# Kernel optimization log

Hardware: AMD Instinct MI355X
Metric: run time of the kernel (lower is better)

The kernel has to match this reference:

```python
import jax, jax.numpy as jnp
import numpy as np


def silu(v):
    return v * jax.nn.sigmoid(v)


def setup_inputs() -> dict:
    key = jax.random.key(0)
    ks = jax.random.split(key, 9)
    B, L, d_model = 2, 2048, 1024
    expand, d_state, d_conv = 2, 16, 4
    d_inner = expand * d_model          # 2048
    dt_rank = (d_model + 15) // 16      # 64 (ceil(d_model/16))
    sc = 0.02
    s = lambda k, shape: (jax.random.normal(k, shape, jnp.float32) * sc)
    A_init = jnp.tile(jnp.arange(1, d_state + 1, dtype=jnp.float32), (d_inner, 1))
    return {
        "x": jax.random.normal(ks[0], (B, L, d_model), jnp.float32),
        "in_proj_w": s(ks[1], (2 * d_inner, d_model)),
        "conv_w": s(ks[2], (d_inner, 1, d_conv)),
        "conv_b": s(ks[3], (d_inner,)),
        "x_proj_w": s(ks[4], (dt_rank + 2 * d_state, d_inner)),
        "dt_proj_w": s(ks[5], (d_inner, dt_rank)),
        "dt_proj_b": s(ks[6], (d_inner,)),
        "A_log": jnp.log(A_init),
        "D": jnp.ones((d_inner,), jnp.float32),
        "out_proj_w": s(ks[7], (d_model, d_inner)),
    }


def _mamba(x, in_proj_w, conv_w, conv_b, x_proj_w, dt_proj_w, dt_proj_b, A_log, D, out_proj_w):
    Bsz, L, d_model = x.shape
    d_inner, _, d_conv = conv_w.shape
    d_state = A_log.shape[1]
    dt_rank = dt_proj_w.shape[1]

    # input projection -> [B, L, 2*d_inner], split into conv branch and gate
    xz = jnp.einsum('bld,ed->ble', x, in_proj_w)
    x_in, z = jnp.split(xz, 2, axis=-1)

    # causal depthwise conv1d over sequence
    xt = jnp.transpose(x_in, (0, 2, 1))                      # [B, d_inner, L]
    xt = jnp.pad(xt, ((0, 0), (0, 0), (d_conv - 1, 0)))
    xc = jax.lax.conv_general_dilated(
        xt, conv_w, window_strides=(1,), padding='VALID',
        dimension_numbers=('NCH', 'OIH', 'NCH'),
        feature_group_count=d_inner)
    xc = xc + conv_b[None, :, None]
    u = silu(jnp.transpose(xc, (0, 2, 1)))                   # [B, L, d_inner]

    # ssm parameter projections
    x_dbl = jnp.einsum('ble,fe->blf', u, x_proj_w)           # [B, L, dt_rank + 2*d_state]
    dt, B_ssm, C_ssm = jnp.split(x_dbl, [dt_rank, dt_rank + d_state], axis=-1)
    delta = jax.nn.softplus(jnp.einsum('blr,er->ble', dt, dt_proj_w) + dt_proj_b)  # [B,L,d_inner]
    A = -jnp.exp(A_log)                                       # [d_inner, d_state]

    # selective scan: h_t = exp(delta_t * A) * h_{t-1} + delta_t * u_t * B_t
    def step(h, inp):
        d_t, B_t, C_t, u_t = inp                              # [B,e],[B,n],[B,n],[B,e]
        dA = jnp.exp(d_t[..., None] * A)                      # [B, d_inner, d_state]
        h = dA * h + (d_t * u_t)[..., None] * B_t[:, None, :]
        y = jnp.einsum('ben,bn->be', h, C_t)
        return h, y

    h0 = jnp.zeros((Bsz, d_inner, d_state), x.dtype)
    scan_in = (jnp.swapaxes(delta, 0, 1), jnp.swapaxes(B_ssm, 0, 1),
               jnp.swapaxes(C_ssm, 0, 1), jnp.swapaxes(u, 0, 1))
    _, ys = jax.lax.scan(step, h0, scan_in)                   # ys: [L, B, d_inner]
    y = jnp.swapaxes(ys, 0, 1) + u * D                        # skip term D*u

    y = y * silu(z)                                           # gate
    return jnp.einsum('ble,de->bld', y, out_proj_w)


def reference(x, in_proj_w, conv_w, conv_b, x_proj_w, dt_proj_w, dt_proj_b, A_log, D, out_proj_w):
    # ResidualMamba: x + Mamba(x)
    return x + _mamba(x, in_proj_w, conv_w, conv_b, x_proj_w,
                      dt_proj_w, dt_proj_b, A_log, D, out_proj_w)
```

## Files before the change

### kernel.cpp

```cpp
#include <hip/hip_runtime.h>
#include <hip/hip_bf16.h>
#include <math.h>

typedef __bf16 bf16;
typedef __attribute__((ext_vector_type(8))) __bf16 bf16x8;
typedef __attribute__((ext_vector_type(4))) __bf16 bf16x4;
typedef __attribute__((ext_vector_type(4))) float  f32x4;

static constexpr int Bsz = 2, L = 2048, DM = 1024, DI = 2048, DS = 16, DTR = 64;
static constexpr int M   = Bsz * L;
static constexpr int NXZ = 2 * DI;
static constexpr int NXD = DTR + 2 * DS;
static constexpr int NC  = 32;
static constexpr int CL  = L / NC;
static constexpr int KS  = 8;
static constexpr float LOG2E = 1.4426950408889634f;

__device__ inline float ex2(float x) { return __builtin_amdgcn_exp2f(x); }

__device__ inline void gload_lds16(const void* g, void* l)
{
    __builtin_amdgcn_global_load_lds(
        (const __attribute__((address_space(1))) void*)g,
        (__attribute__((address_space(3))) void*)l, 16, 0, 0);
}

#define SBAR() { asm volatile("" ::: "memory"); __builtin_amdgcn_s_barrier(); asm volatile("" ::: "memory"); }
#define VMCNT12() asm volatile("s_waitcnt vmcnt(12)" ::: "memory")
#define VMCNT9()  asm volatile("s_waitcnt vmcnt(9)" ::: "memory")
#define VMCNT8()  asm volatile("s_waitcnt vmcnt(8)" ::: "memory")
#define VMCNT6()  asm volatile("s_waitcnt vmcnt(6)" ::: "memory")
#define VMCNT4()  asm volatile("s_waitcnt vmcnt(4)" ::: "memory")
#define VMCNT3()  asm volatile("s_waitcnt vmcnt(3)" ::: "memory")
#define VMCNT0()  asm volatile("s_waitcnt vmcnt(0)" ::: "memory")


static constexpr int C0 = M * DM / 4;
static constexpr int C1 = C0 + NXZ * DM / 4;
static constexpr int C2 = C1 + DM * DI / 4;
static constexpr int C3 = C2 + NXD * DI / 4;
static constexpr int C4 = C3 + DI * DTR / 4;

__global__ __launch_bounds__(256)
void cast_all(const float* __restrict__ s0, const float* __restrict__ s1,
              const float* __restrict__ s2, const float* __restrict__ s3,
              const float* __restrict__ s4,
              bf16* __restrict__ d0, bf16* __restrict__ d1,
              bf16* __restrict__ d2, bf16* __restrict__ d3,
              bf16* __restrict__ d4)
{
    const int i = blockIdx.x * 256 + threadIdx.x;
    const float* s; bf16* d; int off;
    if      (i < C0) { s = s0; d = d0; off = 0;  }
    else if (i < C1) { s = s1; d = d1; off = C0; }
    else if (i < C2) { s = s2; d = d2; off = C1; }
    else if (i < C3) { s = s3; d = d3; off = C2; }
    else             { s = s4; d = d4; off = C3; }
    const int j = i - off;
    float4 v = ((const float4*)s)[j];
    bf16x4 o = {(bf16)v.x, (bf16)v.y, (bf16)v.z, (bf16)v.w};
    ((bf16x4*)d)[j] = o;
}

static constexpr int GK  = DM;
static constexpr int GNT = GK / 64;

__device__ __forceinline__ void stage_half(const bf16* __restrict__ Gbase, int ld,
                                           int kbase, bf16* lds_slot, int tid, int wid)
{
    const int rl = tid >> 2;
    const int ks = ((((tid & 3) - ((tid >> 3) & 3)) & 3) << 3);
#pragma unroll
    for (int i = 0; i < 2; ++i)
        gload_lds16(Gbase + (size_t)(i * 128 + rl) * ld + kbase + ks,
                    lds_slot + i * 4096 + wid * 512);
}

template<int MH>
__device__ __forceinline__ void ldA4(const bf16* As, int abase, bf16x8 af[4])
{
#pragma unroll
    for (int mm = 0; mm < 4; ++mm)
        af[mm] = *(const bf16x8*)(As + abase + (MH * 4 + mm) * 512);
}

__device__ __forceinline__ void ldB4(const bf16* Bs, int bbase, bf16x8 bfr[4])
{
#pragma unroll
    for (int nn = 0; nn < 4; ++nn)
        bfr[nn] = *(const bf16x8*)(Bs + bbase + nn * 512);
}

template<int MH>
__device__ __forceinline__ void mfma16(f32x4 acc[8][4], const bf16x8 af[4],
                                       const bf16x8 bfr[4])
{
#pragma unroll
    for (int mm = 0; mm < 4; ++mm)
#pragma unroll
        for (int nn = 0; nn < 4; ++nn)
            acc[MH * 4 + mm][nn] = __builtin_amdgcn_mfma_f32_16x16x32_bf16(
                af[mm], bfr[nn], acc[MH * 4 + mm][nn], 0, 0, 0);
}

__global__ __launch_bounds__(512, 1)
void gemm256_inproj(const bf16* __restrict__ A, const bf16* __restrict__ Bw,
                    bf16* __restrict__ C)
{
    __shared__ __align__(16) bf16 Asl[4 * 8192];
    __shared__ __align__(16) bf16 Bsl[4 * 8192];

    const int tid  = threadIdx.x;
    const int wid  = tid >> 6;
    const int lane = tid & 63;
    const int wr   = wid >> 2;
    const int wc   = wid & 3;
    const int fr   = lane & 15;
    const int ko16 = lane >> 4;
    const int kx   = (((ko16 + ((fr >> 1) & 3)) & 3) << 3);

    const int bid = blockIdx.x;
    const int wg  = (bid & 7) * 32 + (bid >> 3);
    const int by  = wg >> 4, bx = wg & 15;
    const int row0 = by * 256, col0 = bx * 256;

    const bf16* Ablk = A  + (size_t)row0 * GK;
    const bf16* Bblk = Bw + (size_t)col0 * GK;

    const int abase = (wr * 128 + fr) * 32 + kx;
    const int bbase = (wc * 64 + fr) * 32 + kx;

    f32x4 acc[8][4] = {};
    bf16x8 af[4], bfr[4];

    stage_half(Ablk, GK, 0,       Asl + 0 * 8192, tid, wid);
    stage_half(Bblk, GK, 0,       Bsl + 0 * 8192, tid, wid);
    stage_half(Ablk, GK, 32,      Asl + 1 * 8192, tid, wid);
    stage_half(Bblk, GK, 32,      Bsl + 1 * 8192, tid, wid);
    stage_half(Ablk, GK, 64,      Asl + 2 * 8192, tid, wid);
    stage_half(Bblk, GK, 64,      Bsl + 2 * 8192, tid, wid);
    VMCNT4();
    SBAR();

    for (int t = 0; t < GNT; ++t) {
        const int sk0 = (2 * t) & 3, sk1 = (2 * t + 1) & 3;
        const bf16* As0 = Asl + sk0 * 8192;
        const bf16* As1 = Asl + sk1 * 8192;
        const bf16* Bs0 = Bsl + sk0 * 8192;
        const bf16* Bs1 = Bsl + sk1 * 8192;

        ldA4<0>(As0, abase, af);
        ldB4(Bs0, bbase, bfr);
        if (t + 1 < GNT)
            stage_half(Ablk, GK, (t + 1) * 64 + 32, Asl + ((2 * t + 3) & 3) * 8192, tid, wid);
        SBAR();
        __builtin_amdgcn_s_setprio(1);
        mfma16<0>(acc, af, bfr);
        __builtin_amdgcn_s_setprio(0);
        SBAR();

        ldA4<1>(As0, abase, af);
        if (t + 1 < GNT)
            stage_half(Bblk, GK, (t + 1) * 64 + 32, Bsl + ((2 * t + 3) & 3) * 8192, tid, wid);
        SBAR();
        __builtin_amdgcn_s_setprio(1);
        mfma16<1>(acc, af, bfr);
        __builtin_amdgcn_s_setprio(0);
        SBAR();

        ldA4<0>(As1, abase, af);
        ldB4(Bs1, bbase, bfr);
        if (t + 2 < GNT)
            stage_half(Ablk, GK, (t + 2) * 64, Asl + sk0 * 8192, tid, wid);
        SBAR();
        __builtin_amdgcn_s_setprio(1);
        mfma16<0>(acc, af, bfr);
        __builtin_amdgcn_s_setprio(0);
        SBAR();

        ldA4<1>(As1, abase, af);
        if (t + 2 < GNT)
            stage_half(Bblk, GK, (t + 2) * 64, Bsl + sk0 * 8192, tid, wid);
        SBAR();
        __builtin_amdgcn_s_setprio(1);
        mfma16<1>(acc, af, bfr);
        __builtin_amdgcn_s_setprio(0);
        if (t < GNT - 3) { VMCNT4(); } else { VMCNT0(); }
        SBAR();
    }

    const int r0 = row0 + wr * 128 + (ko16 << 2);
    const int c0 = col0 + wc * 64 + fr;
#pragma unroll
    for (int m = 0; m < 8; ++m)
#pragma unroll
        for (int n = 0; n < 4; ++n)
#pragma unroll
            for (int r = 0; r < 4; ++r)
                C[(size_t)(r0 + m * 16 + r) * NXZ + c0 + n * 16] = (bf16)acc[m][n][r];
}

__global__ __launch_bounds__(256)
void gemm_out(const bf16* __restrict__ A, const bf16* __restrict__ Bw,
              const float* __restrict__ res, float* __restrict__ Cout)
{
    __shared__ __align__(16) bf16 Asl[4][128 * 32];
    __shared__ __align__(16) bf16 Bsl[4][64 * 32];

    const int tid  = threadIdx.x;
    const int bid  = blockIdx.x;
    const int orig = (bid & 7) * 64 + (bid >> 3);
    const int bx   = orig & 15;
    const int by   = orig >> 4;
    const int row0 = by * 128, col0 = bx * 64;

    const int w    = tid >> 6;
    const int lane = tid & 63;
    const int wr   = w >> 1, wc = w & 1;
    const int fr   = lane & 15;
    const int ko   = (((lane >> 4) + ((fr >> 1) & 3)) & 3) << 3;

    f32x4 acc[4][2] = {};

    const int sr  = tid >> 2;
    const int ssk = ((((tid & 3) - ((tid >> 3) & 3)) & 3) << 3);
    const bf16* gA0 = A  + (size_t)(row0 + sr) * NXZ + ssk;
    const bf16* gA1 = A  + (size_t)(row0 + 64 + sr) * NXZ + ssk;
    const bf16* gB0 = Bw + (size_t)(col0 + sr) * DI + ssk;

    const int NT = DI / 32;

#define STAGE_OUT(s, kk) do { \
        gload_lds16(gA0 + (kk), (char*)Asl[s] + w * 1024); \
        gload_lds16(gA1 + (kk), (char*)Asl[s] + 4096 + w * 1024); \
        gload_lds16(gB0 + (kk), (char*)Bsl[s] + w * 1024); } while (0)

    STAGE_OUT(0, 0);
    STAGE_OUT(1, 32);
    STAGE_OUT(2, 64);
    for (int i = 0; i < NT; ++i) {
        const int cur = i & 3;
        if (i + 3 < NT)      { STAGE_OUT((i + 3) & 3, (i + 3) * 32); VMCNT9(); }
        else if (i + 2 < NT) { VMCNT6(); }
        else if (i + 1 < NT) { VMCNT3(); }
        else                 { VMCNT0(); }
        SBAR();

        bf16x8 af[4], bfr[2];
#pragma unroll
        for (int m = 0; m < 4; ++m)
            af[m] = *(const bf16x8*)&Asl[cur][((wr << 6) + m * 16 + fr) * 32 + ko];
#pragma unroll
        for (int n = 0; n < 2; ++n)
            bfr[n] = *(const bf16x8*)&Bsl[cur][((wc << 5) + n * 16 + fr) * 32 + ko];
        __builtin_amdgcn_s_setprio(1);
#pragma unroll
        for (int m = 0; m < 4; ++m)
#pragma unroll
            for (int n = 0; n < 2; ++n)
                acc[m][n] = __builtin_amdgcn_mfma_f32_16x16x32_bf16(
                    af[m], bfr[n], acc[m][n], 0, 0, 0);
        __builtin_amdgcn_s_setprio(0);
        SBAR();
    }
#undef STAGE_OUT

    const int r0 = row0 + (wr << 6) + ((lane >> 4) << 2);
    const int c0 = col0 + (wc << 5) + fr;
#pragma unroll
    for (int m = 0; m < 4; ++m)
#pragma unroll
        for (int n = 0; n < 2; ++n)
#pragma unroll
            for (int r = 0; r < 4; ++r) {
                const int row = r0 + m * 16 + r;
                const int col = c0 + n * 16;
                Cout[(size_t)row * DM + col] =
                    acc[m][n][r] + res[(size_t)row * DM + col];
            }
}

template<int EPI>
__global__ __launch_bounds__(256)
void gemm_bf16(const bf16* __restrict__ A, const bf16* __restrict__ Bw,
               const float* __restrict__ bias, const float* __restrict__ res,
               void* __restrict__ Cout, int N, int K, int lda, int ldc)
{
    __shared__ __align__(16) bf16 Asl[128 * 32];
    __shared__ __align__(16) bf16 Bsl[128 * 32];

    const int tid  = threadIdx.x;
    const int row0 = blockIdx.y * 128;
    const int col0 = blockIdx.x * 128;
    const int w    = tid >> 6;
    const int lane = tid & 63;
    const int wr   = w >> 1, wc = w & 1;
    const int fr   = lane & 15;
    const int ko   = (((lane >> 4) + ((fr >> 1) & 3)) & 3) << 3;

    f32x4 acc[4][4] = {};

    const int sr  = tid >> 2;
    const int ssk = ((((tid & 3) - ((tid >> 3) & 3)) & 3) << 3);
    int brow0 = col0 + sr;       if (brow0 > N - 1) brow0 = N - 1;
    int brow1 = col0 + 64 + sr;  if (brow1 > N - 1) brow1 = N - 1;
    const bf16* gA0 = A  + (size_t)(row0 + sr) * lda + ssk;
    const bf16* gA1 = A  + (size_t)(row0 + 64 + sr) * lda + ssk;
    const bf16* gB0 = Bw + (size_t)brow0 * K + ssk;
    const bf16* gB1 = Bw + (size_t)brow1 * K + ssk;
    char* lA = (char*)Asl + w * 1024;
    char* lB = (char*)Bsl + w * 1024;

    for (int k0 = 0; k0 < K; k0 += 32) {
        gload_lds16(gA0 + k0, lA);
        gload_lds16(gA1 + k0, lA + 4096);
        gload_lds16(gB0 + k0, lB);
        gload_lds16(gB1 + k0, lB + 4096);
        __syncthreads();

        bf16x8 af[4], bfr[4];
#pragma unroll
        for (int m = 0; m < 4; ++m)
            af[m] = *(const bf16x8*)&Asl[((wr << 6) + m * 16 + fr) * 32 + ko];
#pragma unroll
        for (int n = 0; n < 4; ++n)
            bfr[n] = *(const bf16x8*)&Bsl[((wc << 6) + n * 16 + fr) * 32 + ko];
#pragma unroll
        for (int m = 0; m < 4; ++m)
#pragma unroll
            for (int n = 0; n < 4; ++n)
                acc[m][n] = __builtin_amdgcn_mfma_f32_16x16x32_bf16(
                    af[m], bfr[n], acc[m][n], 0, 0, 0);
        __syncthreads();
    }

    const int r0 = row0 + (wr << 6) + ((lane >> 4) << 2);
    const int c0 = col0 + (wc << 6) + fr;
#pragma unroll
    for (int m = 0; m < 4; ++m) {
#pragma unroll
        for (int n = 0; n < 4; ++n) {
            const int col = c0 + n * 16;
            if (col < N) {
#pragma unroll
                for (int r = 0; r < 4; ++r) {
                    const int row = r0 + m * 16 + r;
                    float v = acc[m][n][r];
                    if (EPI == 1) {
                        v += bias[col];
                        v = (v > 20.f) ? v : log1pf(expf(v));
                        ((bf16*)Cout)[(size_t)row * ldc + col] = (bf16)v;
                    } else {
                        ((bf16*)Cout)[(size_t)row * ldc + col] = (bf16)v;
                    }
                }
            }
        }
    }
}

__global__ __launch_bounds__(256)
void gemm_xproj(const bf16* __restrict__ A, const bf16* __restrict__ Bw,
                float* __restrict__ Cpart)
{
    __shared__ __align__(16) bf16 Asl[4][128 * 32];
    __shared__ __align__(16) bf16 Bsl[4][128 * 32];

    const int tid  = threadIdx.x;
    const int row0 = blockIdx.x * 128;
    const int kz   = blockIdx.y;
    const int kb   = kz * (2048 / KS);
    const int w    = tid >> 6;
    const int lane = tid & 63;
    const int wr   = w >> 1, wc = w & 1;
    const int fr   = lane & 15;
    const int ko   = (((lane >> 4) + ((fr >> 1) & 3)) & 3) << 3;

    f32x4 acc[4][4] = {};

    const int sr  = tid >> 2;
    const int ssk = ((((tid & 3) - ((tid >> 3) & 3)) & 3) << 3);
    int brow0 = sr;       if (brow0 > 95) brow0 = 95;
    int brow1 = 64 + sr;  if (brow1 > 95) brow1 = 95;
    const bf16* gA0 = A  + (size_t)(row0 + sr) * DI + kb + ssk;
    const bf16* gA1 = A  + (size_t)(row0 + 64 + sr) * DI + kb + ssk;
    const bf16* gB0 = Bw + (size_t)brow0 * DI + kb + ssk;
    const bf16* gB1 = Bw + (size_t)brow1 * DI + kb + ssk;

    const int NT = (2048 / KS) / 32;

#define STAGE_XP(s, kk) do { \
        gload_lds16(gA0 + (kk), (char*)Asl[s] + w * 1024); \
        gload_lds16(gA1 + (kk), (char*)Asl[s] + 4096 + w * 1024); \
        gload_lds16(gB0 + (kk), (char*)Bsl[s] + w * 1024); \
        gload_lds16(gB1 + (kk), (char*)Bsl[s] + 4096 + w * 1024); } while (0)

    STAGE_XP(0, 0);
    STAGE_XP(1, 32);
    STAGE_XP(2, 64);
    for (int i = 0; i < NT; ++i) {
        const int cur = i & 3;
        if (i + 3 < NT)      { STAGE_XP((i + 3) & 3, (i + 3) * 32); VMCNT12(); }
        else if (i + 2 < NT) { VMCNT8(); }
        else if (i + 1 < NT) { VMCNT4(); }
        else                 { VMCNT0(); }
        SBAR();

        bf16x8 af[4], bfr[4];
#pragma unroll
        for (int m = 0; m < 4; ++m)
            af[m] = *(const bf16x8*)&Asl[cur][((wr << 6) + m * 16 + fr) * 32 + ko];
#pragma unroll
        for (int n = 0; n < 4; ++n)
            bfr[n] = *(const bf16x8*)&Bsl[cur][((wc << 6) + n * 16 + fr) * 32 + ko];
        __builtin_amdgcn_s_setprio(1);
#pragma unroll
        for (int m = 0; m < 4; ++m)
#pragma unroll
            for (int n = 0; n < 4; ++n)
                acc[m][n] = __builtin_amdgcn_mfma_f32_16x16x32_bf16(
                    af[m], bfr[n], acc[m][n], 0, 0, 0);
        __builtin_amdgcn_s_setprio(0);
        SBAR();
    }
#undef STAGE_XP

    const int r0 = (wr << 6) + ((lane >> 4) << 2);
    const int c0 = (wc << 6) + fr;
    float* Cp = Cpart + (size_t)kz * M * 96 + (size_t)row0 * 96;
#pragma unroll
    for (int m = 0; m < 4; ++m) {
#pragma unroll
        for (int n = 0; n < 4; ++n) {
            const int col = c0 + n * 16;
            if (col < 96) {
#pragma unroll
                for (int r = 0; r < 4; ++r)
                    Cp[(size_t)(r0 + m * 16 + r) * 96 + col] = acc[m][n][r];
            }
        }
    }
}

__global__ __launch_bounds__(256)
void reduce_xdbl(const float* __restrict__ part, bf16* __restrict__ xdb)
{
    const int i = blockIdx.x * 256 + threadIdx.x;
    if (i >= M * 96) return;
    float s = 0.f;
#pragma unroll
    for (int k = 0; k < KS; ++k) s += part[(size_t)k * M * 96 + i];
    xdb[i] = (bf16)s;
}

__global__ __launch_bounds__(256)
void conv_silu(const bf16* __restrict__ xzb, const float* __restrict__ cw,
               const float* __restrict__ cb, bf16* __restrict__ u)
{
    const int idx = blockIdx.x * 256 + threadIdx.x;
    const int e   = (idx & 255) * 8;
    const int m   = idx >> 8;
    const int l   = m & (L - 1);

    float wv[8][4];
#pragma unroll
    for (int c = 0; c < 8; ++c) {
        float4 t = *(const float4*)(cw + (size_t)(e + c) * 4);
        wv[c][0] = t.x; wv[c][1] = t.y; wv[c][2] = t.z; wv[c][3] = t.w;
    }
    float acc[8];
    {
        float4 b0 = *(const float4*)(cb + e);
        float4 b1 = *(const float4*)(cb + e + 4);
        acc[0] = b0.x; acc[1] = b0.y; acc[2] = b0.z; acc[3] = b0.w;
        acc[4] = b1.x; acc[5] = b1.y; acc[6] = b1.z; acc[7] = b1.w;
    }
#pragma unroll
    for (int k = 0; k < 4; ++k) {
        if (l + k - 3 >= 0) {
            bf16x8 xv = *(const bf16x8*)&xzb[(size_t)(m + k - 3) * NXZ + e];
#pragma unroll
            for (int c = 0; c < 8; ++c)
                acc[c] = fmaf((float)xv[c], wv[c][k], acc[c]);
        }
    }
    bf16x8 o;
#pragma unroll
    for (int c = 0; c < 8; ++c)
        o[c] = (bf16)(acc[c] / (1.f + __expf(-acc[c])));
    *(bf16x8*)&u[(size_t)m * DI + e] = o;
}

__global__ __launch_bounds__(256)
void scan_pass1(const bf16* __restrict__ xzb, const bf16* __restrict__ ub,
                const bf16* __restrict__ xdb, const float* __restrict__ A_log,
                float* __restrict__ Pend, float* __restrict__ Qend)
{
    __shared__ bf16 sD[CL][256];
    __shared__ bf16 sU[CL][256];
    __shared__ float Bs[CL][DS];
    const int tid = threadIdx.x;
    const int e0 = blockIdx.x * 256;
    const int e  = e0 + tid;
    const int c = blockIdx.y;
    const int b = blockIdx.z;
    const int l0 = c * CL;

#pragma unroll
    for (int it = 0; it < CL / 8; ++it) {
        const int r   = it * 8 + (tid >> 5);
        const int col = (tid & 31) * 8;
        *(bf16x8*)&sD[r][col] = *(const bf16x8*)&xzb[(size_t)(b * L + l0 + r) * NXZ + e0 + col];
        *(bf16x8*)&sU[r][col] = *(const bf16x8*)&ub [(size_t)(b * L + l0 + r) * DI  + e0 + col];
    }
#pragma unroll
    for (int it = 0; it < CL * DS / 256; ++it) {
        const int idx = it * 256 + tid;
        Bs[idx >> 4][idx & 15] =
            (float)xdb[(size_t)(b * L + l0 + (idx >> 4)) * NXD + DTR + (idx & 15)];
    }

    float A2[DS];
#pragma unroll
    for (int q = 0; q < 4; ++q) {
        float4 al = *(const float4*)(A_log + (size_t)e * DS + q * 4);
        A2[q * 4 + 0] = -__expf(al.x) * LOG2E;
        A2[q * 4 + 1] = -__expf(al.y) * LOG2E;
        A2[q * 4 + 2] = -__expf(al.z) * LOG2E;
        A2[q * 4 + 3] = -__expf(al.w) * LOG2E;
    }

    float h[DS];
#pragma unroll
    for (int n = 0; n < DS; ++n) h[n] = 0.f;
    float sumd = 0.f;

    __syncthreads();

#pragma unroll 4
    for (int t = 0; t < CL; ++t) {
        const float dv = (float)sD[t][tid];
        const float uv = (float)sU[t][tid];
        const float du = dv * uv;
        sumd += dv;
#pragma unroll
        for (int n = 0; n < DS; ++n) {
            const float a = ex2(dv * A2[n]);
            h[n] = fmaf(a, h[n], du * Bs[t][n]);
        }
    }

    const size_t o = ((size_t)(c * Bsz + b) * DI + e) * DS;
#pragma unroll
    for (int q = 0; q < 4; ++q) {
        f32x4 P = {ex2(A2[q*4] * sumd), ex2(A2[q*4+1] * sumd),
                   ex2(A2[q*4+2] * sumd), ex2(A2[q*4+3] * sumd)};
        *(f32x4*)(Pend + o + q * 4) = P;
        *(float4*)(Qend + o + q * 4) = make_float4(h[q*4], h[q*4+1], h[q*4+2], h[q*4+3]);
    }
}

__global__ __launch_bounds__(256)
void scan_pass2(const float* __restrict__ Pend, const float* __restrict__ Qend,
                float* __restrict__ H0)
{
    const int g = blockIdx.x * 256 + threadIdx.x;
    const int stride = Bsz * DI * DS;
    float P[NC], Q[NC];
#pragma unroll
    for (int c = 0; c < NC; ++c) {
        P[c] = Pend[(size_t)c * stride + g];
        Q[c] = Qend[(size_t)c * stride + g];
    }
    float h = 0.f;
#pragma unroll
    for (int c = 0; c < NC; ++c) {
        H0[(size_t)c * stride + g] = h;
        h = fmaf(P[c], h, Q[c]);
    }
}

__global__ __launch_bounds__(256)
void scan_pass3(bf16* __restrict__ xzb, const bf16* __restrict__ ub,
                const bf16* __restrict__ xdb, const float* __restrict__ A_log,
                const float* __restrict__ Dp, const float* __restrict__ H0)
{
    __shared__ bf16 sD[CL][256];
    __shared__ bf16 sU[CL][256];
    __shared__ float BCs[CL][2 * DS];
    const int tid = threadIdx.x;
    const int e0 = blockIdx.x * 256;
    const int e  = e0 + tid;
    const int c = blockIdx.y;
    const int b = blockIdx.z;
    const int l0 = c * CL;

#pragma unroll
    for (int it = 0; it < CL / 8; ++it) {
        const int r   = it * 8 + (tid >> 5);
        const int col = (tid & 31) * 8;
        const size_t grow = (size_t)(b * L + l0 + r);
        *(bf16x8*)&sD[r][col] = *(const bf16x8*)&xzb[grow * NXZ + e0 + col];
        *(bf16x8*)&sU[r][col] = *(const bf16x8*)&ub [grow * DI + e0 + col];
    }
#pragma unroll
    for (int it = 0; it < CL * 2 * DS / 256; ++it) {
        const int idx = it * 256 + tid;
        BCs[idx >> 5][idx & 31] =
            (float)xdb[(size_t)(b * L + l0 + (idx >> 5)) * NXD + DTR + (idx & 31)];
    }

    float A2[DS];
#pragma unroll
    for (int q = 0; q < 4; ++q) {
        float4 al = *(const float4*)(A_log + (size_t)e * DS + q * 4);
        A2[q * 4 + 0] = -__expf(al.x) * LOG2E;
        A2[q * 4 + 1] = -__expf(al.y) * LOG2E;
        A2[q * 4 + 2] = -__expf(al.z) * LOG2E;
        A2[q * 4 + 3] = -__expf(al.w) * LOG2E;
    }

    float h[DS];
    const size_t o = (size_t)c * (Bsz * DI * DS) + ((size_t)b * DI + e) * DS;
#pragma unroll
    for (int q = 0; q < 4; ++q) {
        float4 hv = *(const float4*)(H0 + o + q * 4);
        h[q*4] = hv.x; h[q*4+1] = hv.y; h[q*4+2] = hv.z; h[q*4+3] = hv.w;
    }
    const float Dval = Dp[e];

    __syncthreads();

#pragma unroll 4
    for (int t = 0; t < CL; ++t) {
        const float dv = (float)sD[t][tid];
        const float uv = (float)sU[t][tid];
        const float du = dv * uv;
        float y = 0.f;
#pragma unroll
        for (int n = 0; n < DS; ++n) {
            const float a = ex2(dv * A2[n]);
            h[n] = fmaf(a, h[n], du * BCs[t][n]);
            y = fmaf(h[n], BCs[t][DS + n], y);
        }
        sD[t][tid] = (bf16)(y + uv * Dval);
    }

    __syncthreads();
#pragma unroll
    for (int it = 0; it < CL / 8; ++it) {
        const int r   = it * 8 + (tid >> 5);
        const int col = (tid & 31) * 8;
        const size_t grow = (size_t)(b * L + l0 + r);
        bf16x8 zv = *(const bf16x8*)&xzb[grow * NXZ + DI + e0 + col];
        bf16x8 yv = *(bf16x8*)&sD[r][col];
        bf16x8 ov;
#pragma unroll
        for (int j = 0; j < 8; ++j) {
            const float z = (float)zv[j];
            ov[j] = (bf16)((float)yv[j] * (z / (1.f + __expf(-z))));
        }
        *(bf16x8*)&xzb[grow * NXZ + e0 + col] = ov;
    }
}

extern "C" void kernel_launch(void* const* d_in, const int* in_sizes, int n_in,
                              void* d_out, int out_size, void* d_ws, size_t ws_size,
                              hipStream_t stream)
{
    const float* x          = (const float*)d_in[0];
    const float* in_proj_w  = (const float*)d_in[1];
    const float* conv_w     = (const float*)d_in[2];
    const float* conv_b     = (const float*)d_in[3];
    const float* x_proj_w   = (const float*)d_in[4];
    const float* dt_proj_w  = (const float*)d_in[5];
    const float* dt_proj_b  = (const float*)d_in[6];
    const float* A_log      = (const float*)d_in[7];
    const float* Dp         = (const float*)d_in[8];
    const float* out_proj_w = (const float*)d_in[9];
    float* out = (float*)d_out;

    bf16* xzb   = (bf16*)d_ws;
    bf16* ub    = xzb   + (size_t)M * NXZ;
    bf16* xdb   = ub    + (size_t)M * DI;
    bf16* xb    = xdb   + (size_t)M * NXD;
    bf16* wbin  = xb    + (size_t)M * DM;
    bf16* wbout = wbin  + (size_t)NXZ * DM;
    bf16* wbxp  = wbout + (size_t)DM * DI;
    bf16* wbdt  = wbxp  + (size_t)NXD * DI;
    float* Pend = (float*)(wbdt + (size_t)DI * DTR);
    float* Qend = Pend + (size_t)NC * Bsz * DI * DS;
    float* H0   = Qend + (size_t)NC * Bsz * DI * DS;
    float* xpart = Pend;

    const dim3 blk(256);

    cast_all<<<dim3(C4 / 256), blk, 0, stream>>>(
        x, in_proj_w, out_proj_w, x_proj_w, dt_proj_w,
        xb, wbin, wbout, wbxp, wbdt);

    gemm256_inproj<<<dim3(256), dim3(512), 0, stream>>>(xb, wbin, xzb);

    conv_silu<<<dim3(M * (DI / 8) / 256), blk, 0, stream>>>(xzb, conv_w, conv_b, ub);

    gemm_xproj<<<dim3(M / 128, KS), blk, 0, stream>>>(ub, wbxp, xpart);
    reduce_xdbl<<<dim3(M * 96 / 256), blk, 0, stream>>>(xpart, xdb);

    gemm_bf16<1><<<dim3(DI / 128, M / 128), blk, 0, stream>>>(
        xdb, wbdt, dt_proj_b, nullptr, xzb, DI, DTR, NXD, NXZ);

    scan_pass1<<<dim3(DI / 256, NC, Bsz), blk, 0, stream>>>(xzb, ub, xdb, A_log, Pend, Qend);
    scan_pass2<<<dim3(Bsz * DI * DS / 256), blk, 0, stream>>>(Pend, Qend, H0);
    scan_pass3<<<dim3(DI / 256, NC, Bsz), blk, 0, stream>>>(xzb, ub, xdb, A_log, Dp, H0);

    gemm_out<<<dim3(512), blk, 0, stream>>>(xzb, wbout, x, out);
}
```

Measured before the change: 244.3 us.

## Stream u through a register ring instead of LDS in scan passes

Removes the sU shared-memory staging buffer from both scan passes. Each thread now reads u directly from global memory into an 8-deep register ring that is prefetched 8 timesteps ahead. It also adds a min-blocks-per-CU hint of 4 to the launch bounds. The aim is to halve LDS use per block so more blocks fit per CU, and to hide u load latency behind the recurrence. The cost is per-thread strided 2-byte global loads instead of coalesced vector loads, plus tighter register pressure under the occupancy hint.

```diff
diff --git a/kernel.cpp b/kernel.cpp
--- a/kernel.cpp
+++ b/kernel.cpp
@@ -491,13 +491,12 @@
     *(bf16x8*)&u[(size_t)m * DI + e] = o;
 }
 
-__global__ __launch_bounds__(256)
+__global__ __launch_bounds__(256, 4)
 void scan_pass1(const bf16* __restrict__ xzb, const bf16* __restrict__ ub,
                 const bf16* __restrict__ xdb, const float* __restrict__ A_log,
                 float* __restrict__ Pend, float* __restrict__ Qend)
 {
     __shared__ bf16 sD[CL][256];
-    __shared__ bf16 sU[CL][256];
     __shared__ float Bs[CL][DS];
     const int tid = threadIdx.x;
     const int e0 = blockIdx.x * 256;
@@ -511,7 +510,6 @@
         const int r   = it * 8 + (tid >> 5);
         const int col = (tid & 31) * 8;
         *(bf16x8*)&sD[r][col] = *(const bf16x8*)&xzb[(size_t)(b * L + l0 + r) * NXZ + e0 + col];
-        *(bf16x8*)&sU[r][col] = *(const bf16x8*)&ub [(size_t)(b * L + l0 + r) * DI  + e0 + col];
     }
 #pragma unroll
     for (int it = 0; it < CL * DS / 256; ++it) {
@@ -530,6 +528,11 @@
         A2[q * 4 + 3] = -__expf(al.w) * LOG2E;
     }
 
+    const size_t uidx = (size_t)(b * L + l0) * DI + e;
+    bf16 ur[8];
+#pragma unroll
+    for (int j = 0; j < 8; ++j) ur[j] = ub[uidx + (size_t)j * DI];
+
     float h[DS];
 #pragma unroll
     for (int n = 0; n < DS; ++n) h[n] = 0.f;
@@ -537,16 +540,21 @@
 
     __syncthreads();
 
-#pragma unroll 4
-    for (int t = 0; t < CL; ++t) {
-        const float dv = (float)sD[t][tid];
-        const float uv = (float)sU[t][tid];
-        const float du = dv * uv;
-        sumd += dv;
-#pragma unroll
-        for (int n = 0; n < DS; ++n) {
-            const float a = ex2(dv * A2[n]);
-            h[n] = fmaf(a, h[n], du * Bs[t][n]);
+    for (int t8 = 0; t8 < CL; t8 += 8) {
+        const bool more = (t8 + 8 < CL);
+#pragma unroll
+        for (int j = 0; j < 8; ++j) {
+            const int t = t8 + j;
+            const float dv = (float)sD[t][tid];
+            const float uv = (float)ur[j];
+            const float du = dv * uv;
+            sumd += dv;
+#pragma unroll
+            for (int n = 0; n < DS; ++n) {
+                const float a = ex2(dv * A2[n]);
+                h[n] = fmaf(a, h[n], du * Bs[t][n]);
+            }
+            if (more) ur[j] = ub[uidx + (size_t)(t + 8) * DI];
         }
     }
 
@@ -580,13 +588,12 @@
     }
 }
 
-__global__ __launch_bounds__(256)
+__global__ __launch_bounds__(256, 4)
 void scan_pass3(bf16* __restrict__ xzb, const bf16* __restrict__ ub,
                 const bf16* __restrict__ xdb, const float* __restrict__ A_log,
                 const float* __restrict__ Dp, const float* __restrict__ H0)
 {
     __shared__ bf16 sD[CL][256];
-    __shared__ bf16 sU[CL][256];
     __shared__ float BCs[CL][2 * DS];
     const int tid = threadIdx.x;
     const int e0 = blockIdx.x * 256;
@@ -599,9 +606,7 @@
     for (int it = 0; it < CL / 8; ++it) {
         const int r   = it * 8 + (tid >> 5);
         const int col = (tid & 31) * 8;
-        const size_t grow = (size_t)(b * L + l0 + r);
-        *(bf16x8*)&sD[r][col] = *(const bf16x8*)&xzb[grow * NXZ + e0 + col];
-        *(bf16x8*)&sU[r][col] = *(const bf16x8*)&ub [grow * DI + e0 + col];
+        *(bf16x8*)&sD[r][col] = *(const bf16x8*)&xzb[(size_t)(b * L + l0 + r) * NXZ + e0 + col];
     }
 #pragma unroll
     for (int it = 0; it < CL * 2 * DS / 256; ++it) {
@@ -620,6 +625,11 @@
         A2[q * 4 + 3] = -__expf(al.w) * LOG2E;
     }
 
+    const size_t uidx = (size_t)(b * L + l0) * DI + e;
+    bf16 ur[8];
+#pragma unroll
+    for (int j = 0; j < 8; ++j) ur[j] = ub[uidx + (size_t)j * DI];
+
     float h[DS];
     const size_t o = (size_t)c * (Bsz * DI * DS) + ((size_t)b * DI + e) * DS;
 #pragma unroll
@@ -631,19 +641,24 @@
 
     __syncthreads();
 
-#pragma unroll 4
-    for (int t = 0; t < CL; ++t) {
-        const float dv = (float)sD[t][tid];
-        const float uv = (float)sU[t][tid];
-        const float du = dv * uv;
-        float y = 0.f;
-#pragma unroll
-        for (int n = 0; n < DS; ++n) {
-            const float a = ex2(dv * A2[n]);
-            h[n] = fmaf(a, h[n], du * BCs[t][n]);
-            y = fmaf(h[n], BCs[t][DS + n], y);
+    for (int t8 = 0; t8 < CL; t8 += 8) {
+        const bool more = (t8 + 8 < CL);
+#pragma unroll
+        for (int j = 0; j < 8; ++j) {
+            const int t = t8 + j;
+            const float dv = (float)sD[t][tid];
+            const float uv = (float)ur[j];
+            const float du = dv * uv;
+            float y = 0.f;
+#pragma unroll
+            for (int n = 0; n < DS; ++n) {
+                const float a = ex2(dv * A2[n]);
+                h[n] = fmaf(a, h[n], du * BCs[t][n]);
+                y = fmaf(h[n], BCs[t][DS + n], y);
+            }
+            sD[t][tid] = (bf16)(y + uv * Dval);
+            if (more) ur[j] = ub[uidx + (size_t)(t + 8) * DI];
         }
-        sD[t][tid] = (bf16)(y + uv * Dval);
     }
 
     __syncthreads();
```

Result: no change. 248.0 us (+1.5%).
